# Performance work log

Hardware: AMD Instinct MI355X
Metric: run time of the kernel (lower is better)

Reference implementation:

```python
import jax, jax.numpy as jnp
import numpy as np

IN_F, OUT_F, MAX_LEN = 768, 512, 1024
NEG_INF = -9e15

def leaky_relu(x, slope=0.2):
    return jnp.where(x >= 0, x, slope * x)

def setup_inputs() -> dict:
    key = jax.random.key(0)
    k1, k2, k3, k4, k5, k6, k7 = jax.random.split(key, 7)
    B, N = 8, 1024
    h = jax.random.normal(k1, (B, N, IN_F), dtype=jnp.float32)
    adj = jax.random.randint(k2, (B, N, N), 0, 2, dtype=jnp.int32)
    positions = jax.random.randint(k3, (B, N), 0, MAX_LEN, dtype=jnp.int64)
    # learned params (nn.Linear stores weight [out,in]; we keep [in,out] for x@W)
    W = jax.random.normal(k4, (IN_F, OUT_F), dtype=jnp.float32) / np.sqrt(IN_F)
    # a: Linear(2*OUT_F, 1) -> vector of length 2*OUT_F, split into a1 (self) / a2 (neighbor)
    a = jax.random.normal(k5, (2 * OUT_F,), dtype=jnp.float32) / np.sqrt(2 * OUT_F)
    pos_table = jax.random.normal(k6, (MAX_LEN, OUT_F), dtype=jnp.float32) * 0.02
    return {"h": h, "adj": adj, "positions": positions, "W": W, "a": a, "pos_table": pos_table}

def reference(h, adj, positions, W, a, pos_table):
    # Wh: [B,N,Do]
    Wh = jnp.einsum("bnd,do->bno", h, W) + pos_table[positions]
    # additive-attention trick: a([Wh_i ; Wh_j]) = Wh_i@a1 + Wh_j@a2
    a1, a2 = a[:OUT_F], a[OUT_F:]
    f1 = Wh @ a1  # [B,N] score contribution of source (repeat_interleave side)
    f2 = Wh @ a2  # [B,N] score contribution of target (repeat side)
    e = leaky_relu(f1[:, :, None] + f2[:, None, :])  # [B,N,N]
    e = jnp.where(adj > 0, e, NEG_INF)
    attention = jax.nn.softmax(e, axis=-1)  # [B,N,N]
    h_prime = jnp.einsum("bnm,bmo->bno", attention, Wh)  # [B,N,Do]
    return h_prime, attention
```

## Files before the change

### kernel.cpp

```cpp
#include <hip/hip_runtime.h>
#include <stdint.h>

#define BATCH 8
#define NNODE 1024
#define INF 768
#define OUTF 512
#define MTOT (BATCH * NNODE)

typedef __attribute__((ext_vector_type(8))) short short8;
typedef __attribute__((ext_vector_type(4))) short short4v;
typedef __attribute__((ext_vector_type(4))) float floatx4;

__device__ __forceinline__ unsigned short f2bf(float f) {
  union { float f; unsigned u; } v; v.f = f;
  unsigned r = v.u + 0x7fffu + ((v.u >> 16) & 1u);
  return (unsigned short)(r >> 16);
}

__device__ __forceinline__ void gload_lds16(const void* g, void* l) {
  __builtin_amdgcn_global_load_lds(
      (const __attribute__((address_space(1))) void*)g,
      (__attribute__((address_space(3))) void*)l, 16, 0, 0);
}

__global__ __launch_bounds__(256) void prep_kernel(
    const float* __restrict__ h, const float* __restrict__ W,
    short* __restrict__ hbf, short* __restrict__ Wt, float* __restrict__ f12) {
  __shared__ float tile[32][33];
  int bid = blockIdx.x;
  int t = threadIdx.x;
  if (bid < 3072) {
    size_t i = ((size_t)bid * 256 + t) * 8;
    float4 v0 = *(const float4*)&h[i];
    float4 v1 = *(const float4*)&h[i + 4];
    short8 o;
    o[0] = (short)f2bf(v0.x); o[1] = (short)f2bf(v0.y);
    o[2] = (short)f2bf(v0.z); o[3] = (short)f2bf(v0.w);
    o[4] = (short)f2bf(v1.x); o[5] = (short)f2bf(v1.y);
    o[6] = (short)f2bf(v1.z); o[7] = (short)f2bf(v1.w);
    *(short8*)&hbf[i] = o;
    if (bid < 16) {
      float4 z = make_float4(0.f, 0.f, 0.f, 0.f);
      *(float4*)&f12[bid * 1024 + t * 4] = z;
    }
  } else {
    int tb = bid - 3072;
    int o0 = (tb & 15) * 32;
    int k0 = (tb >> 4) * 32;
    int x = t & 31, y = t >> 5;
#pragma unroll
    for (int q = 0; q < 4; ++q) {
      int r = y * 4 + q;
      tile[r][x] = W[(size_t)(k0 + r) * OUTF + o0 + x];
    }
    __syncthreads();
#pragma unroll
    for (int q = 0; q < 4; ++q) {
      int r = y * 4 + q;
      Wt[(size_t)(o0 + r) * INF + k0 + x] = (short)f2bf(tile[x][r]);
    }
  }
}

__global__ __launch_bounds__(512) void gemm1_kernel(
    const short* __restrict__ hbf, const short* __restrict__ Wt,
    const int* __restrict__ positions, const float* __restrict__ pos_table,
    const float* __restrict__ a, float* __restrict__ f12,
    short* __restrict__ Wht) {
  __shared__ short smem[4][8192];
  int bid0 = blockIdx.x;
  int bid = (bid0 & 7) * 32 + (bid0 >> 3);
  int nt = bid & 3, mt = bid >> 2;
  int M0 = mt * 128, N0 = nt * 128;
  int t = threadIdx.x;
  int wv = t >> 6, lane = t & 63;
  int wr = (wv >> 2) * 64, wc = (wv & 3) * 32;
  int l16 = lane & 15, kq = lane >> 4;

  floatx4 acc[4][2] = {};

  auto stage = [&](int buf, int kt) {
#pragma unroll
    for (int i = 0; i < 2; ++i) {
      int q = wv * 64 + lane + i * 512;
      int row = q >> 3;
      int cg = (q & 7) ^ (row & 7);
      gload_lds16(&hbf[(size_t)(M0 + row) * INF + kt * 64 + cg * 8],
                  &smem[buf * 2][(wv * 64 + i * 512) * 8]);
      gload_lds16(&Wt[(size_t)(N0 + row) * INF + kt * 64 + cg * 8],
                  &smem[buf * 2 + 1][(wv * 64 + i * 512) * 8]);
    }
  };

  stage(0, 0);
  __syncthreads();
  int cur = 0;
  for (int kt = 0; kt < 12; ++kt) {
    if (kt < 11) stage(cur ^ 1, kt + 1);
    const short* As = smem[cur * 2];
    const short* Bs = smem[cur * 2 + 1];
#pragma unroll
    for (int ks = 0; ks < 2; ++ks) {
      short8 af[4], bfv[2];
#pragma unroll
      for (int mi = 0; mi < 4; ++mi) {
        int r = wr + mi * 16 + l16;
        af[mi] = *(const short8*)&As[r * 64 + (((ks * 4 + kq) ^ (r & 7)) * 8)];
      }
#pragma unroll
      for (int ni = 0; ni < 2; ++ni) {
        int r = wc + ni * 16 + l16;
        bfv[ni] = *(const short8*)&Bs[r * 64 + (((ks * 4 + kq) ^ (r & 7)) * 8)];
      }
#pragma unroll
      for (int mi = 0; mi < 4; ++mi)
#pragma unroll
        for (int ni = 0; ni < 2; ++ni)
          acc[mi][ni] = __builtin_amdgcn_mfma_f32_16x16x32_bf16(af[mi], bfv[ni], acc[mi][ni], 0, 0, 0);
    }
    __syncthreads();
    cur ^= 1;
  }

  int oc0 = N0 + wc + l16;
  int oc1 = oc0 + 16;
#pragma unroll
  for (int mi = 0; mi < 4; ++mi)
#pragma unroll
    for (int j = 0; j < 4; ++j) {
      int row = M0 + wr + mi * 16 + kq * 4 + j;
      int pos = positions[row];
      acc[mi][0][j] += pos_table[(size_t)pos * OUTF + oc0];
      acc[mi][1][j] += pos_table[(size_t)pos * OUTF + oc1];
    }
  short* T = &smem[0][0];
#pragma unroll
  for (int mi = 0; mi < 4; ++mi)
#pragma unroll
    for (int ni = 0; ni < 2; ++ni)
#pragma unroll
      for (int j = 0; j < 4; ++j)
        T[(wc + ni * 16 + l16) * 136 + wr + mi * 16 + kq * 4 + j] =
            (short)f2bf(acc[mi][ni][j]);
  float a10 = a[oc0], a11 = a[oc1];
  float a20 = a[OUTF + oc0], a21 = a[OUTF + oc1];
  float v1[16], v2[16];
#pragma unroll
  for (int mi = 0; mi < 4; ++mi)
#pragma unroll
    for (int j = 0; j < 4; ++j) {
      v1[mi * 4 + j] = acc[mi][0][j] * a10 + acc[mi][1][j] * a11;
      v2[mi * 4 + j] = acc[mi][0][j] * a20 + acc[mi][1][j] * a21;
    }
#pragma unroll
  for (int mlen = 8; mlen >= 1; mlen >>= 1) {
    bool hi = (l16 & mlen) != 0;
#pragma unroll
    for (int i = 0; i < mlen; ++i) {
      float k1 = hi ? v1[mlen + i] : v1[i];
      float s1 = hi ? v1[i] : v1[mlen + i];
      float k2 = hi ? v2[mlen + i] : v2[i];
      float s2 = hi ? v2[i] : v2[mlen + i];
      v1[i] = k1 + __shfl_xor(s1, mlen);
      v2[i] = k2 + __shfl_xor(s2, mlen);
    }
  }
  {
    int rrow = M0 + wr + (l16 >> 2) * 16 + kq * 4 + (l16 & 3);
    atomicAdd(&f12[rrow], v1[0]);
    atomicAdd(&f12[MTOT + rrow], v2[0]);
  }
  __syncthreads();
  int bb = M0 >> 10, i0 = M0 & 1023;
#pragma unroll
  for (int i = 0; i < 4; ++i) {
    int c = t + i * 512;
    int row = c >> 4;
    int mc = (c & 15) * 8;
    short8 vv = *(const short8*)&T[row * 136 + mc];
    *(short8*)&Wht[((size_t)bb * OUTF + N0 + row) * NNODE + i0 + mc] = vv;
  }
}

__global__ __launch_bounds__(512) void smpv_kernel(
    const float* __restrict__ f12, const int* __restrict__ adj,
    const short* __restrict__ Wht, float* __restrict__ att,
    float* __restrict__ hp) {
  __shared__ short lds[65536];
  short* pbf = lds;
  short* Bbuf0 = lds + 32768;
  short* Bbuf1 = lds + 49152;

  int bid0 = blockIdx.x;
  int b = bid0 & 7, rb = bid0 >> 3;
  int r0 = rb * 32;
  int t = threadIdx.x;
  int wv = t >> 6, lane = t & 63;
  int l16 = lane & 15, kq = lane >> 4;
  const short* Wb = Wht + (size_t)b * OUTF * NNODE;

  auto stageB = [&](short* dst, int kt) {
#pragma unroll
    for (int i = 0; i < 4; ++i) {
      int q = wv * 64 + lane + i * 512;
      int r = q >> 2, s = q & 3;
      int cg = s ^ (r & 3);
      gload_lds16(&Wb[(size_t)r * NNODE + kt * 32 + cg * 8],
                  dst + (wv * 64 + i * 512) * 8);
    }
  };
  stageB(Bbuf0, 0);

  {
    int row = t >> 4, sub = t & 15;
    int gm = b * NNODE + r0 + row;
    float f1v = f12[gm];
    const float* f2b = f12 + MTOT + b * NNODE;
    const int* adjrow = adj + (size_t)gm * NNODE;
    float e[64];
#pragma unroll
    for (int i = 0; i < 16; ++i) {
      int col = sub * 4 + i * 64;
      int4 av = *(const int4*)&adjrow[col];
      float4 fv = *(const float4*)&f2b[col];
      float x;
      x = f1v + fv.x; x = x >= 0.f ? x : 0.2f * x; e[i * 4 + 0] = av.x > 0 ? x : -9e15f;
      x = f1v + fv.y; x = x >= 0.f ? x : 0.2f * x; e[i * 4 + 1] = av.y > 0 ? x : -9e15f;
      x = f1v + fv.z; x = x >= 0.f ? x : 0.2f * x; e[i * 4 + 2] = av.z > 0 ? x : -9e15f;
      x = f1v + fv.w; x = x >= 0.f ? x : 0.2f * x; e[i * 4 + 3] = av.w > 0 ? x : -9e15f;
    }
    float mx = e[0];
#pragma unroll
    for (int i = 1; i < 64; ++i) mx = fmaxf(mx, e[i]);
#pragma unroll
    for (int off = 1; off < 16; off <<= 1) mx = fmaxf(mx, __shfl_xor(mx, off));
    float s = 0.f;
#pragma unroll
    for (int i = 0; i < 64; ++i) { e[i] = expf(e[i] - mx); s += e[i]; }
#pragma unroll
    for (int off = 1; off < 16; off <<= 1) s += __shfl_xor(s, off);
    float inv = 1.f / s;
    float* attrow = att + (size_t)gm * NNODE;
#pragma unroll
    for (int i = 0; i < 16; ++i) {
      int col = sub * 4 + i * 64;
      float4 o = make_float4(e[i * 4] * inv, e[i * 4 + 1] * inv,
                             e[i * 4 + 2] * inv, e[i * 4 + 3] * inv);
      *(float4*)&attrow[col] = o;
      int c = (sub >> 1) + 8 * i;
      short4v pb;
      pb[0] = (short)f2bf(o.x); pb[1] = (short)f2bf(o.y);
      pb[2] = (short)f2bf(o.z); pb[3] = (short)f2bf(o.w);
      *(short4v*)&pbf[row * 1024 + ((c ^ (row & 7)) * 8) + (sub & 1) * 4] = pb;
    }
  }
  __syncthreads();

  int wc = wv * 64;
  floatx4 acc[2][4] = {};
  int cur = 0;
  for (int kt = 0; kt < 32; ++kt) {
    if (kt < 31) stageB(cur ? Bbuf0 : Bbuf1, kt + 1);
    const short* Bsc = cur ? Bbuf1 : Bbuf0;
    short8 af[2], bfv[4];
#pragma unroll
    for (int mi = 0; mi < 2; ++mi) {
      int r = mi * 16 + l16;
      af[mi] = *(const short8*)&pbf[r * 1024 + (((kt * 4 + kq) ^ (r & 7)) * 8)];
    }
#pragma unroll
    for (int ni = 0; ni < 4; ++ni) {
      int r = wc + ni * 16 + l16;
      bfv[ni] = *(const short8*)&Bsc[r * 32 + ((kq ^ (r & 3)) * 8)];
    }
#pragma unroll
    for (int mi = 0; mi < 2; ++mi)
#pragma unroll
      for (int ni = 0; ni < 4; ++ni)
        acc[mi][ni] = __builtin_amdgcn_mfma_f32_16x16x32_bf16(af[mi], bfv[ni], acc[mi][ni], 0, 0, 0);
    __syncthreads();
    cur ^= 1;
  }

#pragma unroll
  for (int mi = 0; mi < 2; ++mi)
#pragma unroll
    for (int j = 0; j < 4; ++j) {
      int grow = b * NNODE + r0 + mi * 16 + kq * 4 + j;
#pragma unroll
      for (int ni = 0; ni < 4; ++ni)
        hp[(size_t)grow * OUTF + wc + ni * 16 + l16] = acc[mi][ni][j];
    }
}

extern "C" void kernel_launch(void* const* d_in, const int* in_sizes, int n_in,
                              void* d_out, int out_size, void* d_ws, size_t ws_size,
                              hipStream_t stream) {
  const float* h = (const float*)d_in[0];
  const int* adj = (const int*)d_in[1];
  const int* positions = (const int*)d_in[2];
  const float* W = (const float*)d_in[3];
  const float* a = (const float*)d_in[4];
  const float* pos_table = (const float*)d_in[5];

  float* hp = (float*)d_out;
  float* att = hp + (size_t)MTOT * OUTF;

  char* ws = (char*)d_ws;
  short* Wt = (short*)ws;
  short* Wht = (short*)(ws + 786432);
  float* f12 = (float*)(ws + 786432 + 8388608);
  short* hbf = (short*)(ws + 786432 + 8388608 + 65536);

  prep_kernel<<<3456, 256, 0, stream>>>(h, W, hbf, Wt, f12);
  gemm1_kernel<<<256, 512, 0, stream>>>(hbf, Wt, positions, pos_table, a, f12, Wht);
  smpv_kernel<<<256, 512, 0, stream>>>(f12, adj, Wht, att, hp);
}
```

Measured before the change: 68.54 us.

## Prefetch two stages ahead with partial vmcnt waits in both GEMM loops

Both MFMA main loops (the projection GEMM and the attention@Wh GEMM) now issue loads two tiles ahead into the double buffer. Each iteration uses an explicit s_waitcnt vmcnt(4) so only the older tile's LDS-direct loads must finish, then a raw s_barrier. The buffer is refilled after a second barrier at the end of the iteration. The aim is to keep one tile of global loads in flight across each iteration instead of draining all of them at every __syncthreads. It relies on hand-counted vmcnt values (4 loads per stage per thread), so any change in load count would break correctness. The second kernel's softmax phase also sits between the two initial prefetches, and its own loads affect the counters.

```diff
diff --git a/kernel.cpp b/kernel.cpp
--- a/kernel.cpp
+++ b/kernel.cpp
@@ -93,12 +93,15 @@
   };
 
   stage(0, 0);
-  __syncthreads();
-  int cur = 0;
+  stage(1, 1);
   for (int kt = 0; kt < 12; ++kt) {
-    if (kt < 11) stage(cur ^ 1, kt + 1);
-    const short* As = smem[cur * 2];
-    const short* Bs = smem[cur * 2 + 1];
+    if (kt + 1 < 12) asm volatile("s_waitcnt vmcnt(4)" ::: "memory");
+    else             asm volatile("s_waitcnt vmcnt(0)" ::: "memory");
+    __builtin_amdgcn_sched_barrier(0);
+    __builtin_amdgcn_s_barrier();
+    asm volatile("" ::: "memory");
+    const short* As = smem[(kt & 1) * 2];
+    const short* Bs = smem[(kt & 1) * 2 + 1];
 #pragma unroll
     for (int ks = 0; ks < 2; ++ks) {
       short8 af[4], bfv[2];
@@ -118,8 +121,10 @@
         for (int ni = 0; ni < 2; ++ni)
           acc[mi][ni] = __builtin_amdgcn_mfma_f32_16x16x32_bf16(af[mi], bfv[ni], acc[mi][ni], 0, 0, 0);
     }
-    __syncthreads();
-    cur ^= 1;
+    asm volatile("" ::: "memory");
+    __builtin_amdgcn_s_barrier();
+    asm volatile("" ::: "memory");
+    if (kt + 2 < 12) stage(kt & 1, kt + 2);
   }
 
   int oc0 = N0 + wc + l16;
@@ -210,6 +215,7 @@
     }
   };
   stageB(Bbuf0, 0);
+  stageB(Bbuf1, 1);
 
   {
     int row = t >> 4, sub = t & 15;
@@ -258,10 +264,13 @@
 
   int wc = wv * 64;
   floatx4 acc[2][4] = {};
-  int cur = 0;
   for (int kt = 0; kt < 32; ++kt) {
-    if (kt < 31) stageB(cur ? Bbuf0 : Bbuf1, kt + 1);
-    const short* Bsc = cur ? Bbuf1 : Bbuf0;
+    if (kt + 1 < 32) asm volatile("s_waitcnt vmcnt(4)" ::: "memory");
+    else             asm volatile("s_waitcnt vmcnt(0)" ::: "memory");
+    __builtin_amdgcn_sched_barrier(0);
+    __builtin_amdgcn_s_barrier();
+    asm volatile("" ::: "memory");
+    const short* Bsc = (kt & 1) ? Bbuf1 : Bbuf0;
     short8 af[2], bfv[4];
 #pragma unroll
     for (int mi = 0; mi < 2; ++mi) {
@@ -278,8 +287,10 @@
 #pragma unroll
       for (int ni = 0; ni < 4; ++ni)
         acc[mi][ni] = __builtin_amdgcn_mfma_f32_16x16x32_bf16(af[mi], bfv[ni], acc[mi][ni], 0, 0, 0);
-    __syncthreads();
-    cur ^= 1;
+    asm volatile("" ::: "memory");
+    __builtin_amdgcn_s_barrier();
+    asm volatile("" ::: "memory");
+    if (kt + 2 < 32) stageB((kt & 1) ? Bbuf1 : Bbuf0, kt + 2);
   }
 
 #pragma unroll
```

After: 59.75 us. 1.15x faster.

## Triple-buffer GEMM K-loops with vmcnt waits and interleave attention stores

Applied to the files above, without the earlier changes.

Both the projection GEMM and the attention-times-Wh GEMM move from double to triple buffering in LDS. Loads run two tiles ahead, and the full __syncthreads is replaced by explicit vmcnt waits plus a single s_barrier per iteration. In the softmax kernel, the fp32 attention-row stores are spread across the K-loop iterations so the large output write overlaps with MFMA work instead of stalling before it. The costs are more LDS per block, which may lower occupancy, and hand-tuned vmcnt counts that must match the exact number of outstanding loads and stores, including the new attention stores.

```diff
diff --git a/kernel.cpp b/kernel.cpp
--- a/kernel.cpp
+++ b/kernel.cpp
@@ -10,6 +10,8 @@
 typedef __attribute__((ext_vector_type(8))) short short8;
 typedef __attribute__((ext_vector_type(4))) short short4v;
 typedef __attribute__((ext_vector_type(4))) float floatx4;
+
+#define WAITVM(N) asm volatile("s_waitcnt vmcnt(" #N ")" ::: "memory")
 
 __device__ __forceinline__ unsigned short f2bf(float f) {
   union { float f; unsigned u; } v; v.f = f;
@@ -67,7 +69,7 @@
     const int* __restrict__ positions, const float* __restrict__ pos_table,
     const float* __restrict__ a, float* __restrict__ f12,
     short* __restrict__ Wht) {
-  __shared__ short smem[4][8192];
+  __shared__ short smem[6][8192];
   int bid0 = blockIdx.x;
   int bid = (bid0 & 7) * 32 + (bid0 >> 3);
   int nt = bid & 3, mt = bid >> 2;
@@ -93,12 +95,21 @@
   };
 
   stage(0, 0);
-  __syncthreads();
-  int cur = 0;
+  stage(1, 1);
+  int cb = 0;
   for (int kt = 0; kt < 12; ++kt) {
-    if (kt < 11) stage(cur ^ 1, kt + 1);
-    const short* As = smem[cur * 2];
-    const short* Bs = smem[cur * 2 + 1];
+    if (kt < 11) WAITVM(4);
+    else         WAITVM(0);
+    __builtin_amdgcn_sched_barrier(0);
+    __builtin_amdgcn_s_barrier();
+    __builtin_amdgcn_sched_barrier(0);
+    if (kt + 2 < 12) {
+      int sb = (cb == 0) ? 2 : cb - 1;
+      stage(sb, kt + 2);
+    }
+    __builtin_amdgcn_sched_barrier(0);
+    const short* As = smem[cb * 2];
+    const short* Bs = smem[cb * 2 + 1];
 #pragma unroll
     for (int ks = 0; ks < 2; ++ks) {
       short8 af[4], bfv[2];
@@ -118,9 +129,9 @@
         for (int ni = 0; ni < 2; ++ni)
           acc[mi][ni] = __builtin_amdgcn_mfma_f32_16x16x32_bf16(af[mi], bfv[ni], acc[mi][ni], 0, 0, 0);
     }
-    __syncthreads();
-    cur ^= 1;
-  }
+    cb = (cb == 2) ? 0 : cb + 1;
+  }
+  __syncthreads();
 
   int oc0 = N0 + wc + l16;
   int oc1 = oc0 + 16;
@@ -186,10 +197,11 @@
     const float* __restrict__ f12, const int* __restrict__ adj,
     const short* __restrict__ Wht, float* __restrict__ att,
     float* __restrict__ hp) {
-  __shared__ short lds[65536];
+  __shared__ short lds[81920];
   short* pbf = lds;
-  short* Bbuf0 = lds + 32768;
-  short* Bbuf1 = lds + 49152;
+  short* Bb0 = lds + 32768;
+  short* Bb1 = lds + 49152;
+  short* Bb2 = lds + 65536;
 
   int bid0 = blockIdx.x;
   int b = bid0 & 7, rb = bid0 >> 3;
@@ -209,15 +221,17 @@
                   dst + (wv * 64 + i * 512) * 8);
     }
   };
-  stageB(Bbuf0, 0);
-
+  stageB(Bb0, 0);
+  stageB(Bb1, 1);
+
+  int row = t >> 4, sub = t & 15;
+  int gm = b * NNODE + r0 + row;
+  float e[64];
+  float inv;
   {
-    int row = t >> 4, sub = t & 15;
-    int gm = b * NNODE + r0 + row;
     float f1v = f12[gm];
     const float* f2b = f12 + MTOT + b * NNODE;
     const int* adjrow = adj + (size_t)gm * NNODE;
-    float e[64];
 #pragma unroll
     for (int i = 0; i < 16; ++i) {
       int col = sub * 4 + i * 64;
@@ -239,29 +253,47 @@
     for (int i = 0; i < 64; ++i) { e[i] = expf(e[i] - mx); s += e[i]; }
 #pragma unroll
     for (int off = 1; off < 16; off <<= 1) s += __shfl_xor(s, off);
-    float inv = 1.f / s;
-    float* attrow = att + (size_t)gm * NNODE;
+    inv = 1.f / s;
 #pragma unroll
     for (int i = 0; i < 16; ++i) {
-      int col = sub * 4 + i * 64;
-      float4 o = make_float4(e[i * 4] * inv, e[i * 4 + 1] * inv,
-                             e[i * 4 + 2] * inv, e[i * 4 + 3] * inv);
-      *(float4*)&attrow[col] = o;
       int c = (sub >> 1) + 8 * i;
       short4v pb;
-      pb[0] = (short)f2bf(o.x); pb[1] = (short)f2bf(o.y);
-      pb[2] = (short)f2bf(o.z); pb[3] = (short)f2bf(o.w);
+      pb[0] = (short)f2bf(e[i * 4 + 0] * inv);
+      pb[1] = (short)f2bf(e[i * 4 + 1] * inv);
+      pb[2] = (short)f2bf(e[i * 4 + 2] * inv);
+      pb[3] = (short)f2bf(e[i * 4 + 3] * inv);
       *(short4v*)&pbf[row * 1024 + ((c ^ (row & 7)) * 8) + (sub & 1) * 4] = pb;
     }
   }
-  __syncthreads();
+  asm volatile("s_waitcnt lgkmcnt(0)" ::: "memory");
+  __builtin_amdgcn_sched_barrier(0);
 
   int wc = wv * 64;
   floatx4 acc[2][4] = {};
-  int cur = 0;
+  float* attrow = att + (size_t)gm * NNODE;
+#pragma unroll 32
   for (int kt = 0; kt < 32; ++kt) {
-    if (kt < 31) stageB(cur ? Bbuf0 : Bbuf1, kt + 1);
-    const short* Bsc = cur ? Bbuf1 : Bbuf0;
+    if (kt == 0)       WAITVM(4);
+    else if (kt == 1)  WAITVM(5);
+    else if (kt == 31) WAITVM(2);
+    else               WAITVM(6);
+    __builtin_amdgcn_sched_barrier(0);
+    __builtin_amdgcn_s_barrier();
+    __builtin_amdgcn_sched_barrier(0);
+    if (kt + 2 < 32) {
+      int sb = (kt + 2) % 3;
+      stageB(sb == 0 ? Bb0 : (sb == 1 ? Bb1 : Bb2), kt + 2);
+    }
+    __builtin_amdgcn_sched_barrier(0);
+    if ((sub >> 3) == (kt & 1)) {
+      int i = kt >> 1;
+      float4 o = make_float4(e[i * 4 + 0] * inv, e[i * 4 + 1] * inv,
+                             e[i * 4 + 2] * inv, e[i * 4 + 3] * inv);
+      *(float4*)&attrow[kt * 32 + (sub & 7) * 4] = o;
+    }
+    __builtin_amdgcn_sched_barrier(0);
+    const int cbi = kt % 3;
+    const short* Bsc = cbi == 0 ? Bb0 : (cbi == 1 ? Bb1 : Bb2);
     short8 af[2], bfv[4];
 #pragma unroll
     for (int mi = 0; mi < 2; ++mi) {
@@ -278,8 +310,6 @@
 #pragma unroll
       for (int ni = 0; ni < 4; ++ni)
         acc[mi][ni] = __builtin_amdgcn_mfma_f32_16x16x32_bf16(af[mi], bfv[ni], acc[mi][ni], 0, 0, 0);
-    __syncthreads();
-    cur ^= 1;
   }
 
 #pragma unroll
```

After: 61.29 us. 1.12x faster.
